# Kernel tuning notes

Hardware: AMD Instinct MI355X
Metric: run time of the kernel (lower is better)

Reference implementation:

```python
import jax, jax.numpy as jnp
import numpy as np

H = 4  # num_heads (hard-coded in module)
RATION = 5


def setup_inputs() -> dict:
    key = jax.random.key(0)
    ks = jax.random.split(key, 14)
    B, T, S, F = 256, 5, 64, 256
    u = 0.05  # keras 'uniform' initializer scale
    d = {}
    d["x"] = jax.random.normal(ks[0], (B, T, S, F), jnp.float32)
    d["atten_bias"] = jax.random.uniform(ks[1], (B, T, S, S), jnp.float32) * 0.1
    d["W_q"] = jax.random.uniform(ks[2], (F, F), jnp.float32, -u, u)
    d["W_v"] = jax.random.uniform(ks[3], (F, F), jnp.float32, -u, u)
    d["W_o"] = jax.random.uniform(ks[4], (F, F), jnp.float32, -u, u)
    d["u_t"] = jax.random.uniform(ks[5], (T,), jnp.float32, -u, u)
    d["dis"] = jax.random.uniform(ks[6], (T, S, S), jnp.float32, -u, u)
    # keep sigma away from 0 to avoid blowing up the Gaussian prior
    d["sigma"] = jax.random.uniform(ks[7], (T, S, 1), jnp.float32, 0.5, 1.0)
    # SE block: fc1 Dense(T*RATION, relu, he_normal), fc2 Dense(T, sigmoid)
    d["fc1_w"] = jax.random.normal(ks[8], (T, T * RATION), jnp.float32) * np.sqrt(2.0 / T).astype(np.float32)
    d["fc1_b"] = jnp.zeros((T * RATION,), jnp.float32)
    d["fc2_w"] = jax.random.normal(ks[9], (T * RATION, T), jnp.float32) * np.sqrt(2.0 / (T * RATION)).astype(np.float32)
    d["fc2_b"] = jnp.zeros((T,), jnp.float32)
    d["bili_w"] = jax.random.uniform(ks[10], (1,), jnp.float32, -u, u)
    return d


def _se_block(o, fc1_w, fc1_b, fc2_w, fc2_b, bili_w):
    # o: [B,T,S,F] -> transpose to [B,S,F,T]; "channel" axis is T
    xt = jnp.transpose(o, (0, 2, 3, 1))
    avg = jnp.mean(xt, axis=(1, 2))  # [B,T]
    mx = jnp.max(xt, axis=(1, 2))    # [B,T]
    se1 = jax.nn.sigmoid(jax.nn.relu(avg @ fc1_w + fc1_b) @ fc2_w + fc2_b)
    se2 = jax.nn.sigmoid(jax.nn.relu(mx @ fc1_w + fc1_b) @ fc2_w + fc2_b)
    w = bili_w  # shape (1,)
    se = (1.0 - w) * se1 + w * se2   # [B,T]
    out = xt * se[:, None, None, :]
    return jnp.transpose(out, (0, 3, 1, 2))  # back to [B,T,S,F]


def reference(x, atten_bias, W_q, W_v, W_o, u_t, dis, sigma, fc1_w, fc1_b, fc2_w, fc2_b, bili_w):
    B, T, S, F = x.shape
    Fh = F // H
    # q, v: project then reshape (row-major split, exactly as TF reshape)
    q = (x @ W_q).reshape(-1, T, S, Fh)          # [H*B, T, S, Fh]
    v = (x @ W_v).reshape(-1, T, S, Fh)          # [H*B, T, S, Fh]
    # k: contract time with u_t, then [B,F,S] -> [H*B, Fh, S]
    k = jnp.einsum('t,btsf->bsf', u_t, x)        # [B, S, F]
    k = jnp.transpose(k, (0, 2, 1)).reshape(-1, Fh, S)  # [H*B, Fh, S]
    score = jnp.einsum('btsf,bfc->btsc', q, k) / jnp.sqrt(jnp.asarray(Fh, x.dtype))
    score = jax.nn.sigmoid(score)                # [H*B, T, S, S]
    score = score - jnp.tile(atten_bias, (H, 1, 1, 1))
    # learned spatial Gaussian prior, broadcast over batch
    prior = (1.0 / (jnp.sqrt(2.0 * jnp.pi) * sigma)) * jnp.exp(-dis ** 2 / (2.0 * sigma ** 2))
    score = score * prior
    # Dropout(0.3) is identity at inference
    score = jnp.sum(score, axis=-2)              # [H*B, T, S]
    atten = v * score[..., None]                 # [H*B, T, S, Fh]
    o = atten.reshape(-1, T, S, F) @ W_o         # [B, T, S, F]
    o = _se_block(o, fc1_w, fc1_b, fc2_w, fc2_b, bili_w)
    return o + x
```

## Files before the change

### kernel.cpp

```cpp
#include <hip/hip_runtime.h>


typedef unsigned short ushort_t;
typedef __attribute__((ext_vector_type(8))) short bf16x8;
typedef __attribute__((ext_vector_type(4))) float f32x4;

__device__ inline ushort_t f2bf(float f) {
  unsigned u = __float_as_uint(f);
  return (ushort_t)((u + 0x7FFFu + ((u >> 16) & 1u)) >> 16);
}
__device__ inline float bflo(unsigned u) { return __uint_as_float(u << 16); }
__device__ inline float bfhi(unsigned u) { return __uint_as_float(u & 0xFFFF0000u); }
__device__ inline uint4 pack8(float4 a, float4 b) {
  uint4 r;
  r.x = (unsigned)f2bf(a.x) | ((unsigned)f2bf(a.y) << 16);
  r.y = (unsigned)f2bf(a.z) | ((unsigned)f2bf(a.w) << 16);
  r.z = (unsigned)f2bf(b.x) | ((unsigned)f2bf(b.y) << 16);
  r.w = (unsigned)f2bf(b.z) | ((unsigned)f2bf(b.w) << 16);
  return r;
}
__device__ inline void gload16(const ushort_t* g, ushort_t* l) {
  __builtin_amdgcn_global_load_lds((const __attribute__((address_space(1))) void*)g,
                                   (__attribute__((address_space(3))) void*)l, 16, 0, 0);
}

__global__ __launch_bounds__(256, 4) void prep_kernel(
    const float* __restrict__ x, const float* __restrict__ u,
    const float* __restrict__ Wq, const float* __restrict__ Wv,
    const float* __restrict__ Wo, const float* __restrict__ dis,
    const float* __restrict__ sigma, const float* __restrict__ bias,
    ushort_t* __restrict__ Wt, float* __restrict__ prior,
    float* __restrict__ bps, ushort_t* __restrict__ kout,
    ushort_t* __restrict__ xb) {
  __shared__ float red[4][64];
  const int blk = blockIdx.x, tid = threadIdx.x;
  if (blk < 768) {
    int id = blk * 256 + tid;
    int mat = id >> 16, rem = id & 65535;
    int n = rem >> 8, k = rem & 255;
    const float* W = mat == 0 ? Wq : (mat == 1 ? Wv : Wo);
    Wt[id] = f2bf(W[k * 256 + n]);
  } else if (blk < 848) {
    int i = (blk - 768) * 256 + tid;
    int ts = i >> 6;
    float sg = sigma[ts];
    float d = dis[i];
    prior[i] = 0.3989422804014327f / sg * __expf(-d * d / (2.f * sg * sg));
  } else if (blk < 2128) {
    int b2 = blk - 848;
    int t = b2 % 5;
    const float* bp = bias + (size_t)b2 * 4096;
    int c = tid & 63, sg_ = tid >> 6;
    float sum = 0.f;
    for (int s = sg_ * 16; s < sg_ * 16 + 16; ++s) {
      float sgm = sigma[t * 64 + s];
      float d = dis[t * 4096 + s * 64 + c];
      float pr = 0.3989422804014327f / sgm * __expf(-d * d / (2.f * sgm * sgm));
      sum += bp[s * 64 + c] * pr;
    }
    red[sg_][c] = sum;
    __syncthreads();
    if (tid < 64)
      bps[(size_t)b2 * 64 + tid] = red[0][tid] + red[1][tid] + red[2][tid] + red[3][tid];
  } else {
    int i = (blk - 2128) * 256 + tid;
    size_t j = (size_t)i * 8;
    int b = (int)(j >> 14);
    int off = (int)(j & 16383);
    const float* xp = x + (size_t)b * 81920 + off;
    ushort_t* xq = xb + (size_t)b * 81920 + off;
    float u0 = u[0], u1 = u[1], u2 = u[2], u3 = u[3], u4 = u[4];
    float4 lo[5], hi[5];
#pragma unroll
    for (int t = 0; t < 5; ++t) {
      lo[t] = *(const float4*)(xp + t * 16384);
      hi[t] = *(const float4*)(xp + t * 16384 + 4);
    }
#pragma unroll
    for (int t = 0; t < 5; ++t)
      *(uint4*)(xq + t * 16384) = pack8(lo[t], hi[t]);
    float4 rl, rh;
    rl.x = u0*lo[0].x + u1*lo[1].x + u2*lo[2].x + u3*lo[3].x + u4*lo[4].x;
    rl.y = u0*lo[0].y + u1*lo[1].y + u2*lo[2].y + u3*lo[3].y + u4*lo[4].y;
    rl.z = u0*lo[0].z + u1*lo[1].z + u2*lo[2].z + u3*lo[3].z + u4*lo[4].z;
    rl.w = u0*lo[0].w + u1*lo[1].w + u2*lo[2].w + u3*lo[3].w + u4*lo[4].w;
    rh.x = u0*hi[0].x + u1*hi[1].x + u2*hi[2].x + u3*hi[3].x + u4*hi[4].x;
    rh.y = u0*hi[0].y + u1*hi[1].y + u2*hi[2].y + u3*hi[3].y + u4*hi[4].y;
    rh.z = u0*hi[0].z + u1*hi[1].z + u2*hi[2].z + u3*hi[3].z + u4*hi[4].z;
    rh.w = u0*hi[0].w + u1*hi[1].w + u2*hi[2].w + u3*hi[3].w + u4*hi[4].w;
    *(uint4*)(kout + j) = pack8(rl, rh);
  }
}

__global__ __launch_bounds__(256) void qscore(const ushort_t* __restrict__ xb,
                                              const ushort_t* __restrict__ Wtq,
                                              const ushort_t* __restrict__ kbuf,
                                              const float* __restrict__ prior,
                                              const float* __restrict__ bps,
                                              float* __restrict__ ssum) {
  __shared__ __align__(16) char smem[46080];
  ushort_t* As_ = (ushort_t*)smem;
  ushort_t* Bs_ = (ushort_t*)(smem + 10240);
  ushort_t* qlds = (ushort_t*)smem;
  const int n = blockIdx.x;
  const int tid = threadIdx.x;
  const int lane = tid & 63, w = tid >> 6;
  const int cl = lane & 15, ql = lane >> 4, l7 = lane & 7;
  const ushort_t* A = xb + (size_t)n * 20480;

  const int c = w * 16 + cl;
  const int nb = n & 255;
  const ushort_t* kbp = kbuf + (size_t)(n >> 2) * 16384 + (n & 3) * 64;
  bf16x8 kfr0 = *(const bf16x8*)(kbp + c * 256 + ql * 8);
  bf16x8 kfr1 = *(const bf16x8*)(kbp + c * 256 + ql * 8 + 32);

  f32x4 acc[5][4];
#pragma unroll
  for (int mi = 0; mi < 5; ++mi)
#pragma unroll
    for (int ni = 0; ni < 4; ++ni) acc[mi][ni] = (f32x4){0.f, 0.f, 0.f, 0.f};

  for (int t4 = 0; t4 < 4; ++t4) {
    const int k0 = t4 * 64;
    if (t4) __syncthreads();
#pragma unroll
    for (int l = 0; l < 3; ++l) {
      int i = l * 256 + tid;
      if (i < 640) {
        int r = i >> 3, cc = i & 7;
        uint4 v = *(const uint4*)(A + (size_t)r * 256 + k0 + cc * 8);
        *(uint4*)&As_[r * 64 + ((cc ^ (r & 7)) * 8)] = v;
      }
    }
#pragma unroll
    for (int l = 0; l < 8; ++l) {
      int i = l * 256 + tid;
      int nn = i >> 3, cc = i & 7;
      uint4 v = *(const uint4*)(Wtq + (size_t)nn * 256 + k0 + cc * 8);
      *(uint4*)&Bs_[nn * 64 + ((cc ^ (nn & 7)) * 8)] = v;
    }
    __syncthreads();
#pragma unroll
    for (int kk = 0; kk < 2; ++kk) {
      const int offk = (((kk << 2) | ql) ^ l7) * 8;
      bf16x8 bfr[4];
#pragma unroll
      for (int ni = 0; ni < 4; ++ni)
        bfr[ni] = *(const bf16x8*)&Bs_[(w * 64 + ni * 16 + cl) * 64 + offk];
#pragma unroll
      for (int mi = 0; mi < 5; ++mi) {
        bf16x8 afr = *(const bf16x8*)&As_[(mi * 16 + cl) * 64 + offk];
#pragma unroll
        for (int ni = 0; ni < 4; ++ni)
          acc[mi][ni] = __builtin_amdgcn_mfma_f32_16x16x32_bf16(afr, bfr[ni], acc[mi][ni], 0, 0, 0);
      }
    }
  }
  __syncthreads();
#pragma unroll
  for (int mi = 0; mi < 5; ++mi)
#pragma unroll
    for (int ni = 0; ni < 4; ++ni)
#pragma unroll
      for (int rr = 0; rr < 4; ++rr)
        qlds[(mi * 64 + 16 * ql + 4 * rr + w) * 72 + ni * 16 + cl] = f2bf(acc[mi][ni][rr]);
  __syncthreads();

#pragma unroll
  for (int t = 0; t < 5; ++t) {
    f32x4 sacc[4];
#pragma unroll
    for (int si = 0; si < 4; ++si) {
      bf16x8 a0 = *(const bf16x8*)&qlds[(t * 64 + si * 16 + cl) * 72 + ql * 8];
      bf16x8 a1 = *(const bf16x8*)&qlds[(t * 64 + si * 16 + cl) * 72 + ql * 8 + 32];
      f32x4 z = (f32x4){0.f, 0.f, 0.f, 0.f};
      z = __builtin_amdgcn_mfma_f32_16x16x32_bf16(a0, kfr0, z, 0, 0, 0);
      z = __builtin_amdgcn_mfma_f32_16x16x32_bf16(a1, kfr1, z, 0, 0, 0);
      sacc[si] = z;
    }
    const float* pp = prior + t * 4096;
    float colsum = 0.f;
#pragma unroll
    for (int si = 0; si < 4; ++si) {
#pragma unroll
      for (int r = 0; r < 4; ++r) {
        int s = si * 16 + ql * 4 + r;
        float sg = 1.f / (1.f + __expf(-sacc[si][r] * 0.125f));
        colsum += sg * pp[s * 64 + c];
      }
    }
    colsum += __shfl_xor(colsum, 16);
    colsum += __shfl_xor(colsum, 32);
    if (ql == 0)
      ssum[(size_t)n * 320 + t * 64 + c] = colsum - bps[((size_t)nb * 5 + t) * 64 + c];
  }
}

__global__ __launch_bounds__(512, 4) void vo_gemm(
    const ushort_t* __restrict__ xb, const ushort_t* __restrict__ Wtv,
    const ushort_t* __restrict__ Wto, const float* __restrict__ ssum,
    ushort_t* __restrict__ ob, float* __restrict__ ravg,
    float* __restrict__ rmax) {
  __shared__ __align__(16) ushort_t As_[64 * 64];
  __shared__ __align__(16) ushort_t Bs_[256 * 64];
  __shared__ __align__(16) ushort_t Vs_[64 * 256];
  __shared__ float redS[8], redM[8];
  const int tid = threadIdx.x;
  const int lane = tid & 63;
  const int w = tid >> 6, wr = w >> 2, wc = w & 3;
  const int g = blockIdx.x;
  const int row0 = g * 64;
  const int cl = lane & 15, ql = lane >> 4, l7 = lane & 7;

  f32x4 acc[2][4];
#pragma unroll
  for (int mi = 0; mi < 2; ++mi)
#pragma unroll
    for (int ni = 0; ni < 4; ++ni) acc[mi][ni] = (f32x4){0.f, 0.f, 0.f, 0.f};

  for (int t = 0; t < 4; ++t) {
    const int k0 = t * 64;
    if (t) __syncthreads();
    {
      int i = tid;
      int r = i >> 3, cpos = i & 7, csrc = cpos ^ (r & 7);
      gload16(xb + (size_t)(row0 + r) * 256 + k0 + csrc * 8, &As_[(w * 64) * 8]);
    }
#pragma unroll
    for (int l = 0; l < 4; ++l) {
      int i = l * 512 + tid;
      int n = i >> 3, cpos = i & 7, csrc = cpos ^ (n & 7);
      gload16(Wtv + (size_t)n * 256 + k0 + csrc * 8, &Bs_[(l * 512 + w * 64) * 8]);
    }
    __syncthreads();
#pragma unroll
    for (int kk = 0; kk < 2; ++kk) {
      const int offk = (((kk << 2) | ql) ^ l7) * 8;
      bf16x8 bfr[4], afr[2];
#pragma unroll
      for (int ni = 0; ni < 4; ++ni)
        bfr[ni] = *(const bf16x8*)&Bs_[(wc * 64 + ni * 16 + cl) * 64 + offk];
#pragma unroll
      for (int mi = 0; mi < 2; ++mi)
        afr[mi] = *(const bf16x8*)&As_[(wr * 32 + mi * 16 + cl) * 64 + offk];
#pragma unroll
      for (int mi = 0; mi < 2; ++mi)
#pragma unroll
        for (int ni = 0; ni < 4; ++ni)
          acc[mi][ni] = __builtin_amdgcn_mfma_f32_16x16x32_bf16(afr[mi], bfr[ni], acc[mi][ni], 0, 0, 0);
    }
  }
#pragma unroll
  for (int mi = 0; mi < 2; ++mi) {
    float sc[4];
#pragma unroll
    for (int r = 0; r < 4; ++r)
      sc[r] = ssum[(size_t)(row0 + wr * 32 + mi * 16 + ql * 4 + r) * 4 + wc];
#pragma unroll
    for (int ni = 0; ni < 4; ++ni) {
      int col = wc * 64 + ni * 16 + cl;
#pragma unroll
      for (int r = 0; r < 4; ++r) {
        int row = wr * 32 + mi * 16 + ql * 4 + r;
        int ch = (col >> 3) ^ (row & 31);
        Vs_[row * 256 + ch * 8 + (col & 7)] = f2bf(acc[mi][ni][r] * sc[r]);
      }
    }
  }
  __syncthreads();

#pragma unroll
  for (int mi = 0; mi < 2; ++mi)
#pragma unroll
    for (int ni = 0; ni < 4; ++ni) acc[mi][ni] = (f32x4){0.f, 0.f, 0.f, 0.f};
  for (int t = 0; t < 4; ++t) {
    const int k0 = t * 64;
    if (t) __syncthreads();
#pragma unroll
    for (int l = 0; l < 4; ++l) {
      int i = l * 512 + tid;
      int n = i >> 3, cpos = i & 7, csrc = cpos ^ (n & 7);
      gload16(Wto + (size_t)n * 256 + k0 + csrc * 8, &Bs_[(l * 512 + w * 64) * 8]);
    }
    __syncthreads();
#pragma unroll
    for (int kk = 0; kk < 2; ++kk) {
      const int offk = (((kk << 2) | ql) ^ l7) * 8;
      const int ch = t * 8 + kk * 4 + ql;
      bf16x8 bfr[4], afr[2];
#pragma unroll
      for (int ni = 0; ni < 4; ++ni)
        bfr[ni] = *(const bf16x8*)&Bs_[(wc * 64 + ni * 16 + cl) * 64 + offk];
#pragma unroll
      for (int mi = 0; mi < 2; ++mi) {
        int row = wr * 32 + mi * 16 + cl;
        afr[mi] = *(const bf16x8*)&Vs_[row * 256 + (ch ^ (row & 31)) * 8];
      }
#pragma unroll
      for (int mi = 0; mi < 2; ++mi)
#pragma unroll
        for (int ni = 0; ni < 4; ++ni)
          acc[mi][ni] = __builtin_amdgcn_mfma_f32_16x16x32_bf16(afr[mi], bfr[ni], acc[mi][ni], 0, 0, 0);
    }
  }
  float lsum = 0.f, lmax = -3.4e38f;
#pragma unroll
  for (int mi = 0; mi < 2; ++mi)
#pragma unroll
    for (int ni = 0; ni < 4; ++ni) {
      int col = wc * 64 + ni * 16 + cl;
#pragma unroll
      for (int r = 0; r < 4; ++r) {
        int row = row0 + wr * 32 + mi * 16 + ql * 4 + r;
        float f = acc[mi][ni][r];
        ob[(size_t)row * 256 + col] = f2bf(f);
        lsum += f; lmax = fmaxf(lmax, f);
      }
    }
#pragma unroll
  for (int off = 32; off; off >>= 1) {
    lsum += __shfl_xor(lsum, off);
    lmax = fmaxf(lmax, __shfl_xor(lmax, off));
  }
  if (lane == 0) { redS[w] = lsum; redM[w] = lmax; }
  __syncthreads();
  if (tid == 0) {
    float s = 0.f, m = -3.4e38f;
#pragma unroll
    for (int i = 0; i < 8; ++i) { s += redS[i]; m = fmaxf(m, redM[i]); }
    ravg[g] = s * (1.f / 16384.f);
    rmax[g] = m;
  }
}

__global__ __launch_bounds__(256) void final_kernel(
    const ushort_t* __restrict__ xb, const ushort_t* __restrict__ ob,
    const float* __restrict__ ravg, const float* __restrict__ rmax,
    const float* __restrict__ fc1w, const float* __restrict__ fc1b,
    const float* __restrict__ fc2w, const float* __restrict__ fc2b,
    const float* __restrict__ bili, float* __restrict__ out) {
  __shared__ float sse;
  int i = blockIdx.x * 256 + threadIdx.x;
  size_t j = (size_t)i * 4;
  int bt = (int)(j >> 14);
  uint2 uo = *(const uint2*)(ob + j);
  uint2 ux = *(const uint2*)(xb + j);
  if (threadIdx.x == 0) {
    int b = bt / 5, t = bt % 5;
    float avg[5], mx[5];
    for (int tt = 0; tt < 5; ++tt) { avg[tt] = ravg[b * 5 + tt]; mx[tt] = rmax[b * 5 + tt]; }
    float w = bili[0];
    float s12[2];
    for (int p = 0; p < 2; ++p) {
      const float* in = p == 0 ? avg : mx;
      float a = fc2b[t];
      for (int jj = 0; jj < 25; ++jj) {
        float hh = fc1b[jj];
        for (int tt = 0; tt < 5; ++tt) hh += in[tt] * fc1w[tt * 25 + jj];
        a += fmaxf(hh, 0.f) * fc2w[jj * 5 + t];
      }
      s12[p] = 1.f / (1.f + __expf(-a));
    }
    sse = (1.f - w) * s12[0] + w * s12[1];
  }
  __syncthreads();
  float s = sse;
  float4 r = {bflo(uo.x) * s + bflo(ux.x), bfhi(uo.x) * s + bfhi(ux.x),
              bflo(uo.y) * s + bflo(ux.y), bfhi(uo.y) * s + bfhi(ux.y)};
  *(float4*)(out + j) = r;
}

extern "C" void kernel_launch(void* const* d_in, const int* in_sizes, int n_in,
                              void* d_out, int out_size, void* d_ws, size_t ws_size,
                              hipStream_t stream) {
  const float* x     = (const float*)d_in[0];
  const float* bias  = (const float*)d_in[1];
  const float* Wq    = (const float*)d_in[2];
  const float* Wv    = (const float*)d_in[3];
  const float* Wo    = (const float*)d_in[4];
  const float* u_t   = (const float*)d_in[5];
  const float* dis   = (const float*)d_in[6];
  const float* sigma = (const float*)d_in[7];
  const float* fc1w  = (const float*)d_in[8];
  const float* fc1b  = (const float*)d_in[9];
  const float* fc2w  = (const float*)d_in[10];
  const float* fc2b  = (const float*)d_in[11];
  const float* bili  = (const float*)d_in[12];
  float* out = (float*)d_out;

  char* wsb = (char*)d_ws;
  ushort_t* xbuf = (ushort_t*)wsb;             wsb += 41943040;
  ushort_t* qvb  = (ushort_t*)wsb;             wsb += 41943040;
  ushort_t* kb   = (ushort_t*)wsb;             wsb += 8388608;
  ushort_t* Wt   = (ushort_t*)wsb;             wsb += 393216;
  float*    ssum = (float*)wsb;                wsb += 1310720;
  float*    prior= (float*)wsb;                wsb += 81920;
  float*    bps  = (float*)wsb;                wsb += 327680;
  float*    ravg = (float*)wsb;                wsb += 5120;
  float*    rmax = (float*)wsb;                wsb += 5120;

  prep_kernel<<<4176, 256, 0, stream>>>(x, u_t, Wq, Wv, Wo, dis, sigma, bias,
                                        Wt, prior, bps, kb, xbuf);
  qscore<<<1024, 256, 0, stream>>>(xbuf, Wt, kb, prior, bps, ssum);
  vo_gemm<<<1280, 512, 0, stream>>>(xbuf, Wt + 65536, Wt + 131072, ssum,
                                    qvb, ravg, rmax);
  final_kernel<<<20480, 256, 0, stream>>>(xbuf, qvb, ravg, rmax,
                                          fc1w, fc1b, fc2w, fc2b, bili, out);
}
```

Before: 143.4 us.

## Fuse SE block and residual into V/O GEMM with one block per batch

Merges the V/O projection GEMM and the final SE-scale-plus-residual kernel into a single kernel, where each block handles one batch element across all five time steps. The block computes the per-time avg/max reduction and the SE MLP in shared memory, then reads back its own output tile to apply the scale and add x. This removes a kernel launch and the global round trip of the avg/max statistics. In exchange the grid shrinks from 1280 to 256 blocks, and each block processes its tiles serially, which reduces parallelism.

```diff
diff --git a/kernel.cpp b/kernel.cpp
--- a/kernel.cpp
+++ b/kernel.cpp
@@ -196,178 +196,185 @@
   }
 }
 
-__global__ __launch_bounds__(512, 4) void vo_gemm(
+__global__ __launch_bounds__(512, 2) void vof_gemm(
     const ushort_t* __restrict__ xb, const ushort_t* __restrict__ Wtv,
     const ushort_t* __restrict__ Wto, const float* __restrict__ ssum,
-    ushort_t* __restrict__ ob, float* __restrict__ ravg,
-    float* __restrict__ rmax) {
+    ushort_t* __restrict__ ob, const float* __restrict__ fc1w,
+    const float* __restrict__ fc1b, const float* __restrict__ fc2w,
+    const float* __restrict__ fc2b, const float* __restrict__ bili,
+    float* __restrict__ out) {
   __shared__ __align__(16) ushort_t As_[64 * 64];
   __shared__ __align__(16) ushort_t Bs_[256 * 64];
   __shared__ __align__(16) ushort_t Vs_[64 * 256];
   __shared__ float redS[8], redM[8];
+  __shared__ float seAvg[5], seMax[5], seBC[5];
   const int tid = threadIdx.x;
   const int lane = tid & 63;
   const int w = tid >> 6, wr = w >> 2, wc = w & 3;
-  const int g = blockIdx.x;
-  const int row0 = g * 64;
+  const int b = blockIdx.x;
   const int cl = lane & 15, ql = lane >> 4, l7 = lane & 7;
 
-  f32x4 acc[2][4];
-#pragma unroll
-  for (int mi = 0; mi < 2; ++mi)
-#pragma unroll
-    for (int ni = 0; ni < 4; ++ni) acc[mi][ni] = (f32x4){0.f, 0.f, 0.f, 0.f};
-
-  for (int t = 0; t < 4; ++t) {
-    const int k0 = t * 64;
-    if (t) __syncthreads();
-    {
-      int i = tid;
-      int r = i >> 3, cpos = i & 7, csrc = cpos ^ (r & 7);
-      gload16(xb + (size_t)(row0 + r) * 256 + k0 + csrc * 8, &As_[(w * 64) * 8]);
-    }
-#pragma unroll
-    for (int l = 0; l < 4; ++l) {
-      int i = l * 512 + tid;
-      int n = i >> 3, cpos = i & 7, csrc = cpos ^ (n & 7);
-      gload16(Wtv + (size_t)n * 256 + k0 + csrc * 8, &Bs_[(l * 512 + w * 64) * 8]);
+  for (int tg = 0; tg < 5; ++tg) {
+    const int row0 = b * 320 + tg * 64;
+    f32x4 acc[2][4];
+#pragma unroll
+    for (int mi = 0; mi < 2; ++mi)
+#pragma unroll
+      for (int ni = 0; ni < 4; ++ni) acc[mi][ni] = (f32x4){0.f, 0.f, 0.f, 0.f};
+
+    for (int t = 0; t < 4; ++t) {
+      const int k0 = t * 64;
+      if (t || tg) __syncthreads();
+      {
+        int i = tid;
+        int r = i >> 3, cpos = i & 7, csrc = cpos ^ (r & 7);
+        gload16(xb + (size_t)(row0 + r) * 256 + k0 + csrc * 8, &As_[(w * 64) * 8]);
+      }
+#pragma unroll
+      for (int l = 0; l < 4; ++l) {
+        int i = l * 512 + tid;
+        int n = i >> 3, cpos = i & 7, csrc = cpos ^ (n & 7);
+        gload16(Wtv + (size_t)n * 256 + k0 + csrc * 8, &Bs_[(l * 512 + w * 64) * 8]);
+      }
+      __syncthreads();
+#pragma unroll
+      for (int kk = 0; kk < 2; ++kk) {
+        const int offk = (((kk << 2) | ql) ^ l7) * 8;
+        bf16x8 bfr[4], afr[2];
+#pragma unroll
+        for (int ni = 0; ni < 4; ++ni)
+          bfr[ni] = *(const bf16x8*)&Bs_[(wc * 64 + ni * 16 + cl) * 64 + offk];
+#pragma unroll
+        for (int mi = 0; mi < 2; ++mi)
+          afr[mi] = *(const bf16x8*)&As_[(wr * 32 + mi * 16 + cl) * 64 + offk];
+#pragma unroll
+        for (int mi = 0; mi < 2; ++mi)
+#pragma unroll
+          for (int ni = 0; ni < 4; ++ni)
+            acc[mi][ni] = __builtin_amdgcn_mfma_f32_16x16x32_bf16(afr[mi], bfr[ni], acc[mi][ni], 0, 0, 0);
+      }
+    }
+#pragma unroll
+    for (int mi = 0; mi < 2; ++mi) {
+      float sc[4];
+#pragma unroll
+      for (int r = 0; r < 4; ++r)
+        sc[r] = ssum[(size_t)(row0 + wr * 32 + mi * 16 + ql * 4 + r) * 4 + wc];
+#pragma unroll
+      for (int ni = 0; ni < 4; ++ni) {
+        int col = wc * 64 + ni * 16 + cl;
+#pragma unroll
+        for (int r = 0; r < 4; ++r) {
+          int row = wr * 32 + mi * 16 + ql * 4 + r;
+          int ch = (col >> 3) ^ (row & 31);
+          Vs_[row * 256 + ch * 8 + (col & 7)] = f2bf(acc[mi][ni][r] * sc[r]);
+        }
+      }
     }
     __syncthreads();
-#pragma unroll
-    for (int kk = 0; kk < 2; ++kk) {
-      const int offk = (((kk << 2) | ql) ^ l7) * 8;
-      bf16x8 bfr[4], afr[2];
-#pragma unroll
-      for (int ni = 0; ni < 4; ++ni)
-        bfr[ni] = *(const bf16x8*)&Bs_[(wc * 64 + ni * 16 + cl) * 64 + offk];
-#pragma unroll
-      for (int mi = 0; mi < 2; ++mi)
-        afr[mi] = *(const bf16x8*)&As_[(wr * 32 + mi * 16 + cl) * 64 + offk];
-#pragma unroll
-      for (int mi = 0; mi < 2; ++mi)
+
+#pragma unroll
+    for (int mi = 0; mi < 2; ++mi)
+#pragma unroll
+      for (int ni = 0; ni < 4; ++ni) acc[mi][ni] = (f32x4){0.f, 0.f, 0.f, 0.f};
+    for (int t = 0; t < 4; ++t) {
+      const int k0 = t * 64;
+      if (t) __syncthreads();
+#pragma unroll
+      for (int l = 0; l < 4; ++l) {
+        int i = l * 512 + tid;
+        int n = i >> 3, cpos = i & 7, csrc = cpos ^ (n & 7);
+        gload16(Wto + (size_t)n * 256 + k0 + csrc * 8, &Bs_[(l * 512 + w * 64) * 8]);
+      }
+      __syncthreads();
+#pragma unroll
+      for (int kk = 0; kk < 2; ++kk) {
+        const int offk = (((kk << 2) | ql) ^ l7) * 8;
+        const int ch = t * 8 + kk * 4 + ql;
+        bf16x8 bfr[4], afr[2];
 #pragma unroll
         for (int ni = 0; ni < 4; ++ni)
-          acc[mi][ni] = __builtin_amdgcn_mfma_f32_16x16x32_bf16(afr[mi], bfr[ni], acc[mi][ni], 0, 0, 0);
-    }
-  }
-#pragma unroll
-  for (int mi = 0; mi < 2; ++mi) {
-    float sc[4];
-#pragma unroll
-    for (int r = 0; r < 4; ++r)
-      sc[r] = ssum[(size_t)(row0 + wr * 32 + mi * 16 + ql * 4 + r) * 4 + wc];
-#pragma unroll
-    for (int ni = 0; ni < 4; ++ni) {
-      int col = wc * 64 + ni * 16 + cl;
-#pragma unroll
-      for (int r = 0; r < 4; ++r) {
-        int row = wr * 32 + mi * 16 + ql * 4 + r;
-        int ch = (col >> 3) ^ (row & 31);
-        Vs_[row * 256 + ch * 8 + (col & 7)] = f2bf(acc[mi][ni][r] * sc[r]);
-      }
-    }
-  }
-  __syncthreads();
-
-#pragma unroll
-  for (int mi = 0; mi < 2; ++mi)
-#pragma unroll
-    for (int ni = 0; ni < 4; ++ni) acc[mi][ni] = (f32x4){0.f, 0.f, 0.f, 0.f};
-  for (int t = 0; t < 4; ++t) {
-    const int k0 = t * 64;
-    if (t) __syncthreads();
-#pragma unroll
-    for (int l = 0; l < 4; ++l) {
-      int i = l * 512 + tid;
-      int n = i >> 3, cpos = i & 7, csrc = cpos ^ (n & 7);
-      gload16(Wto + (size_t)n * 256 + k0 + csrc * 8, &Bs_[(l * 512 + w * 64) * 8]);
-    }
+          bfr[ni] = *(const bf16x8*)&Bs_[(wc * 64 + ni * 16 + cl) * 64 + offk];
+#pragma unroll
+        for (int mi = 0; mi < 2; ++mi) {
+          int row = wr * 32 + mi * 16 + cl;
+          afr[mi] = *(const bf16x8*)&Vs_[row * 256 + (ch ^ (row & 31)) * 8];
+        }
+#pragma unroll
+        for (int mi = 0; mi < 2; ++mi)
+#pragma unroll
+          for (int ni = 0; ni < 4; ++ni)
+            acc[mi][ni] = __builtin_amdgcn_mfma_f32_16x16x32_bf16(afr[mi], bfr[ni], acc[mi][ni], 0, 0, 0);
+      }
+    }
+    float lsum = 0.f, lmax = -3.4e38f;
+#pragma unroll
+    for (int mi = 0; mi < 2; ++mi)
+#pragma unroll
+      for (int ni = 0; ni < 4; ++ni) {
+        int col = wc * 64 + ni * 16 + cl;
+#pragma unroll
+        for (int r = 0; r < 4; ++r) {
+          int row = row0 + wr * 32 + mi * 16 + ql * 4 + r;
+          float f = acc[mi][ni][r];
+          ob[(size_t)row * 256 + col] = f2bf(f);
+          lsum += f; lmax = fmaxf(lmax, f);
+        }
+      }
+#pragma unroll
+    for (int off = 32; off; off >>= 1) {
+      lsum += __shfl_xor(lsum, off);
+      lmax = fmaxf(lmax, __shfl_xor(lmax, off));
+    }
+    if (lane == 0) { redS[w] = lsum; redM[w] = lmax; }
     __syncthreads();
-#pragma unroll
-    for (int kk = 0; kk < 2; ++kk) {
-      const int offk = (((kk << 2) | ql) ^ l7) * 8;
-      const int ch = t * 8 + kk * 4 + ql;
-      bf16x8 bfr[4], afr[2];
-#pragma unroll
-      for (int ni = 0; ni < 4; ++ni)
-        bfr[ni] = *(const bf16x8*)&Bs_[(wc * 64 + ni * 16 + cl) * 64 + offk];
-#pragma unroll
-      for (int mi = 0; mi < 2; ++mi) {
-        int row = wr * 32 + mi * 16 + cl;
-        afr[mi] = *(const bf16x8*)&Vs_[row * 256 + (ch ^ (row & 31)) * 8];
-      }
-#pragma unroll
-      for (int mi = 0; mi < 2; ++mi)
-#pragma unroll
-        for (int ni = 0; ni < 4; ++ni)
-          acc[mi][ni] = __builtin_amdgcn_mfma_f32_16x16x32_bf16(afr[mi], bfr[ni], acc[mi][ni], 0, 0, 0);
-    }
-  }
-  float lsum = 0.f, lmax = -3.4e38f;
-#pragma unroll
-  for (int mi = 0; mi < 2; ++mi)
-#pragma unroll
-    for (int ni = 0; ni < 4; ++ni) {
-      int col = wc * 64 + ni * 16 + cl;
-#pragma unroll
-      for (int r = 0; r < 4; ++r) {
-        int row = row0 + wr * 32 + mi * 16 + ql * 4 + r;
-        float f = acc[mi][ni][r];
-        ob[(size_t)row * 256 + col] = f2bf(f);
-        lsum += f; lmax = fmaxf(lmax, f);
-      }
-    }
-#pragma unroll
-  for (int off = 32; off; off >>= 1) {
-    lsum += __shfl_xor(lsum, off);
-    lmax = fmaxf(lmax, __shfl_xor(lmax, off));
-  }
-  if (lane == 0) { redS[w] = lsum; redM[w] = lmax; }
+    if (tid == 0) {
+      float s = 0.f, m = -3.4e38f;
+#pragma unroll
+      for (int i = 0; i < 8; ++i) { s += redS[i]; m = fmaxf(m, redM[i]); }
+      seAvg[tg] = s * (1.f / 16384.f);
+      seMax[tg] = m;
+    }
+  }
   __syncthreads();
   if (tid == 0) {
-    float s = 0.f, m = -3.4e38f;
-#pragma unroll
-    for (int i = 0; i < 8; ++i) { s += redS[i]; m = fmaxf(m, redM[i]); }
-    ravg[g] = s * (1.f / 16384.f);
-    rmax[g] = m;
-  }
-}
-
-__global__ __launch_bounds__(256) void final_kernel(
-    const ushort_t* __restrict__ xb, const ushort_t* __restrict__ ob,
-    const float* __restrict__ ravg, const float* __restrict__ rmax,
-    const float* __restrict__ fc1w, const float* __restrict__ fc1b,
-    const float* __restrict__ fc2w, const float* __restrict__ fc2b,
-    const float* __restrict__ bili, float* __restrict__ out) {
-  __shared__ float sse;
-  int i = blockIdx.x * 256 + threadIdx.x;
-  size_t j = (size_t)i * 4;
-  int bt = (int)(j >> 14);
-  uint2 uo = *(const uint2*)(ob + j);
-  uint2 ux = *(const uint2*)(xb + j);
-  if (threadIdx.x == 0) {
-    int b = bt / 5, t = bt % 5;
-    float avg[5], mx[5];
-    for (int tt = 0; tt < 5; ++tt) { avg[tt] = ravg[b * 5 + tt]; mx[tt] = rmax[b * 5 + tt]; }
-    float w = bili[0];
-    float s12[2];
+    float w_ = bili[0];
+    float s12[2][5];
+#pragma unroll
     for (int p = 0; p < 2; ++p) {
-      const float* in = p == 0 ? avg : mx;
-      float a = fc2b[t];
+      const float* in = p == 0 ? seAvg : seMax;
+      float h[25];
       for (int jj = 0; jj < 25; ++jj) {
         float hh = fc1b[jj];
         for (int tt = 0; tt < 5; ++tt) hh += in[tt] * fc1w[tt * 25 + jj];
-        a += fmaxf(hh, 0.f) * fc2w[jj * 5 + t];
-      }
-      s12[p] = 1.f / (1.f + __expf(-a));
-    }
-    sse = (1.f - w) * s12[0] + w * s12[1];
+        h[jj] = fmaxf(hh, 0.f);
+      }
+      for (int t = 0; t < 5; ++t) {
+        float a = fc2b[t];
+        for (int jj = 0; jj < 25; ++jj) a += h[jj] * fc2w[jj * 5 + t];
+        s12[p][t] = 1.f / (1.f + __expf(-a));
+      }
+    }
+    for (int t = 0; t < 5; ++t)
+      seBC[t] = (1.f - w_) * s12[0][t] + w_ * s12[1][t];
   }
   __syncthreads();
-  float s = sse;
-  float4 r = {bflo(uo.x) * s + bflo(ux.x), bfhi(uo.x) * s + bfhi(ux.x),
-              bflo(uo.y) * s + bflo(ux.y), bfhi(uo.y) * s + bfhi(ux.y)};
-  *(float4*)(out + j) = r;
+
+  for (int cch = 0; cch < 20; ++cch) {
+    int chunk = cch * 512 + tid;
+    int e = chunk * 8;
+    int row = e >> 8;
+    float s = seBC[row >> 6];
+    size_t ge = (size_t)b * 81920 + e;
+    uint4 uo = *(const uint4*)(ob + ge);
+    uint4 ux = *(const uint4*)(xb + ge);
+    float4 r0 = {bflo(uo.x) * s + bflo(ux.x), bfhi(uo.x) * s + bfhi(ux.x),
+                 bflo(uo.y) * s + bflo(ux.y), bfhi(uo.y) * s + bfhi(ux.y)};
+    float4 r1 = {bflo(uo.z) * s + bflo(ux.z), bfhi(uo.z) * s + bfhi(ux.z),
+                 bflo(uo.w) * s + bflo(ux.w), bfhi(uo.w) * s + bfhi(ux.w)};
+    *(float4*)(out + ge) = r0;
+    *(float4*)(out + ge + 4) = r1;
+  }
 }
 
 extern "C" void kernel_launch(void* const* d_in, const int* in_sizes, int n_in,
@@ -390,20 +397,16 @@
 
   char* wsb = (char*)d_ws;
   ushort_t* xbuf = (ushort_t*)wsb;             wsb += 41943040;
-  ushort_t* qvb  = (ushort_t*)wsb;             wsb += 41943040;
+  ushort_t* obuf = (ushort_t*)wsb;             wsb += 41943040;
   ushort_t* kb   = (ushort_t*)wsb;             wsb += 8388608;
   ushort_t* Wt   = (ushort_t*)wsb;             wsb += 393216;
   float*    ssum = (float*)wsb;                wsb += 1310720;
   float*    prior= (float*)wsb;                wsb += 81920;
   float*    bps  = (float*)wsb;                wsb += 327680;
-  float*    ravg = (float*)wsb;                wsb += 5120;
-  float*    rmax = (float*)wsb;                wsb += 5120;
 
   prep_kernel<<<4176, 256, 0, stream>>>(x, u_t, Wq, Wv, Wo, dis, sigma, bias,
                                         Wt, prior, bps, kb, xbuf);
   qscore<<<1024, 256, 0, stream>>>(xbuf, Wt, kb, prior, bps, ssum);
-  vo_gemm<<<1280, 512, 0, stream>>>(xbuf, Wt + 65536, Wt + 131072, ssum,
-                                    qvb, ravg, rmax);
-  final_kernel<<<20480, 256, 0, stream>>>(xbuf, qvb, ravg, rmax,
-                                          fc1w, fc1b, fc2w, fc2b, bili, out);
-}
+  vof_gemm<<<256, 512, 0, stream>>>(xbuf, Wt + 65536, Wt + 131072, ssum, obuf,
+                                    fc1w, fc1b, fc2w, fc2b, bili, out);
+}
```

Result: slower. 170.7 us (+19.0%).
